# Performance work log

Measured on AMD Instinct MI355X. Metric: run time of the kernel, lower is better.

## Reference

```python
import math
import jax, jax.numpy as jnp
import numpy as np

N_TOKENS = 131072
D_MODEL = 1024
NUM_EXPERT = 64
SWITCH_EPS = 0.1
CAP_RATE = 1.2  # training capacity factor


def setup_inputs() -> dict:
    key = jax.random.key(0)
    k1, k2, k3, k4 = jax.random.split(key, 4)
    inp = jax.random.normal(k1, (N_TOKENS, D_MODEL), dtype=jnp.float32)
    W = jax.random.normal(k2, (D_MODEL, NUM_EXPERT), dtype=jnp.float32) * (1.0 / math.sqrt(D_MODEL))
    b = jax.random.normal(k3, (NUM_EXPERT,), dtype=jnp.float32) * 0.01
    noise = jax.random.uniform(k4, (N_TOKENS, NUM_EXPERT), dtype=jnp.float32)
    return {"inp": inp, "W": W, "b": b, "noise": noise}


def reference(inp, W, b, noise):
    n_tokens = inp.shape[0]
    # gate projection + training-time noise injection (noise in [1-eps, 1+eps])
    score = inp @ W + b
    score = score + (noise * (2.0 * SWITCH_EPS) + (1.0 - SWITCH_EPS))
    score = jax.nn.softmax(score.astype(jnp.float32), axis=-1)  # [N, E]

    # top-1 selection
    top1_idx = jnp.argmax(score, axis=-1)  # [N] int
    top1_score = jnp.take_along_axis(score, top1_idx[:, None], axis=-1)  # [N, 1]
    top1_score = top1_score.astype(inp.dtype)

    # capacity-limited pruning: keep first `capacity` tokens per expert (in order)
    capacity = math.ceil(CAP_RATE * n_tokens / NUM_EXPERT)  # static
    onehot = jax.nn.one_hot(top1_idx, NUM_EXPERT, dtype=jnp.int32)  # [N, E]
    # rank of each token within its expert (0-based, tokens in arrival order)
    rank = jnp.sum(jnp.cumsum(onehot, axis=0) * onehot, axis=-1) - 1  # [N]
    pruned_idx = jnp.where(rank < capacity, top1_idx, -1)  # [N]

    # load-balancing loss over valid (non-pruned) assignments
    valid = pruned_idx > -1
    n_valid = jnp.sum(valid).astype(jnp.float32)
    safe_idx = jnp.where(valid, pruned_idx, 0)
    counts = jnp.zeros((NUM_EXPERT,), dtype=jnp.float32).at[safe_idx].add(valid.astype(jnp.float32))
    fraction_expert = counts / n_valid
    prob_expert = jnp.sum(score, axis=0) / n_valid
    loss = jnp.sum(fraction_expert * prob_expert) * NUM_EXPERT

    return pruned_idx[:, None], top1_score, loss
```

## Files before the change

kernel.cpp:

```cpp
#include <hip/hip_runtime.h>
#include <stdint.h>

#define NTOK   131072
#define DM     1024
#define NE     64
#define TB     64
#define NBLK   2048
#define BK     32
#define NCHUNK 32
#define CAP    2458
#define EPG    16

__device__ __forceinline__ void gload_lds16(const float* g, float* l) {
    __builtin_amdgcn_global_load_lds(
        (const __attribute__((address_space(1))) void*)g,
        (__attribute__((address_space(3))) void*)l, 16, 0, 0);
}

__global__ __launch_bounds__(256, 8)
void gate_kernel(const float* __restrict__ A, const float* __restrict__ W,
                 const float* __restrict__ bias, const float* __restrict__ noise,
                 float* __restrict__ out, int* __restrict__ pk,
                 int* __restrict__ histg, float* __restrict__ colpart)
{
    __shared__ float asA[2][TB][BK];
    __shared__ float smax[TB][5];
    __shared__ float ssum[TB][5];
    __shared__ int   sidx[TB][5];

    const int tid  = threadIdx.x;
    const int lane = tid & 63;
    const int wv   = __builtin_amdgcn_readfirstlane(tid >> 6);
    const int g16  = wv << 4;
    const int blk  = blockIdx.x;
    const int tokBase = blk * TB;
    const int token   = tokBase + lane;

    float acc[EPG];
#pragma unroll
    for (int e = 0; e < EPG; ++e) acc[e] = 0.f;

    const int sl = (lane & 7) ^ ((lane >> 3) & 7);
    const float* gsrc = A + (size_t)(tokBase + wv * 16 + (lane >> 3)) * DM + sl * 4;
    float* lb[2] = { &asA[0][wv * 16][0], &asA[1][wv * 16][0] };

    gload_lds16(gsrc,          lb[0]);
    gload_lds16(gsrc + 8 * DM, lb[0] + 8 * BK);

#pragma unroll 1
    for (int c = 0; c < NCHUNK; ++c) {
        const int cur = c & 1;
        __builtin_amdgcn_s_barrier();
        asm volatile("" ::: "memory");
        if (c + 1 < NCHUNK) {
            const float* gn = gsrc + (size_t)(c + 1) * BK;
            float* ln = lb[cur ^ 1];
            gload_lds16(gn,          ln);
            gload_lds16(gn + 8 * DM, ln + 8 * BK);
            asm volatile("s_waitcnt vmcnt(2)" ::: "memory");
        } else {
            asm volatile("s_waitcnt vmcnt(0)" ::: "memory");
        }
        __builtin_amdgcn_sched_barrier(0);
        __builtin_amdgcn_s_barrier();
        asm volatile("" ::: "memory");

        const float* arow = &asA[cur][lane][0];
        const int k0 = c * BK;
#pragma unroll
        for (int q = 0; q < 8; ++q) {
            const float4 xq = *(const float4*)(arow + ((q ^ (lane & 7)) << 2));
            const float xs[4] = {xq.x, xq.y, xq.z, xq.w};
#pragma unroll
            for (int kk = 0; kk < 4; ++kk) {
                const float x = xs[kk];
                const float* wrow = W + (size_t)(k0 + q * 4 + kk) * NE + g16;
#pragma unroll
                for (int e = 0; e < EPG; ++e)
                    acc[e] = fmaf(x, wrow[e], acc[e]);
            }
        }
    }
    __syncthreads();

    const float* nrow = noise + (size_t)token * NE + g16;
    const float* brow = bias + g16;
#pragma unroll
    for (int q = 0; q < 4; ++q) {
        const float4 nv = ((const float4*)nrow)[q];
        acc[q * 4 + 0] += brow[q * 4 + 0] + nv.x * 0.2f + 0.9f;
        acc[q * 4 + 1] += brow[q * 4 + 1] + nv.y * 0.2f + 0.9f;
        acc[q * 4 + 2] += brow[q * 4 + 2] + nv.z * 0.2f + 0.9f;
        acc[q * 4 + 3] += brow[q * 4 + 3] + nv.w * 0.2f + 0.9f;
    }

    float lm = acc[0]; int li = 0;
#pragma unroll
    for (int e = 1; e < EPG; ++e)
        if (acc[e] > lm) { lm = acc[e]; li = e; }
    smax[lane][wv] = lm;
    sidx[lane][wv] = g16 + li;
    __syncthreads();

    float M = smax[lane][0]; int bi = sidx[lane][0];
#pragma unroll
    for (int g2 = 1; g2 < 4; ++g2) {
        const float m2 = smax[lane][g2];
        if (m2 > M) { M = m2; bi = sidx[lane][g2]; }
    }

    float s = 0.f;
#pragma unroll
    for (int e = 0; e < EPG; ++e) { acc[e] = __expf(acc[e] - M); s += acc[e]; }
    ssum[lane][wv] = s;
    __syncthreads();
    const float denom = ssum[lane][0] + ssum[lane][1] + ssum[lane][2] + ssum[lane][3];
    const float inv = 1.0f / denom;
#pragma unroll
    for (int e = 0; e < EPG; ++e) acc[e] *= inv;

    if (wv == 0) out[NTOK + token] = inv;

#define XSTAGE(M_)                                                       \
    {                                                                    \
        const bool up_ = (lane & (M_)) != 0;                             \
        _Pragma("unroll")                                                \
        for (int j = 0; j < (M_); ++j) {                                 \
            const float a_ = acc[j], b_ = acc[j + (M_)];                 \
            const float r_ = __shfl_xor(up_ ? a_ : b_, (M_), 64);        \
            acc[j] = (up_ ? b_ : a_) + r_;                               \
        }                                                                \
    }
    XSTAGE(8) XSTAGE(4) XSTAGE(2) XSTAGE(1)
#undef XSTAGE
    float cs = acc[0];
    cs += __shfl_xor(cs, 16, 64);
    cs += __shfl_xor(cs, 32, 64);
    if (lane < EPG) colpart[blk * NE + g16 + lane] = cs;

    if (wv == 0) {
        const uint64_t below = (1ull << lane) - 1ull;
        int lrank = 0, h = 0;
#pragma unroll 1
        for (int e = 0; e < NE; ++e) {
            const uint64_t mb = __ballot(bi == e);
            if (bi == e)   lrank = (int)__popcll(mb & below);
            if (lane == e) h = (int)__popcll(mb);
        }
        pk[token] = bi | (lrank << 6);
        histg[blk * NE + lane] = h;
    }
}

__global__ __launch_bounds__(256)
void scan_kernel(int* __restrict__ hist, const float* __restrict__ colpart,
                 int* __restrict__ totals, float* __restrict__ colsums)
{
    __shared__ int   wtot[4];
    __shared__ float wcs[4];
    const int e    = blockIdx.x;
    const int t    = threadIdx.x;
    const int lane = t & 63;
    const int w    = t >> 6;
    const int b0   = t * 8;

    int h[8]; int s = 0; float csl = 0.f;
#pragma unroll
    for (int i = 0; i < 8; ++i) {
        h[i]  = hist[(b0 + i) * NE + e];
        csl  += colpart[(b0 + i) * NE + e];
        s    += h[i];
    }
    int inc = s;
#pragma unroll
    for (int d = 1; d < 64; d <<= 1) {
        const int v = __shfl_up(inc, d, 64);
        if (lane >= d) inc += v;
    }
    float wsum = csl;
#pragma unroll
    for (int m = 32; m; m >>= 1) wsum += __shfl_xor(wsum, m, 64);
    if (lane == 63) wtot[w] = inc;
    if (lane == 0)  wcs[w]  = wsum;
    __syncthreads();

    int base = 0;
#pragma unroll
    for (int ww = 0; ww < 4; ++ww) base += (ww < w) ? wtot[ww] : 0;
    int run = base + inc - s;
#pragma unroll
    for (int i = 0; i < 8; ++i) { hist[(b0 + i) * NE + e] = run; run += h[i]; }

    if (t == 0) {
        totals[e]  = wtot[0] + wtot[1] + wtot[2] + wtot[3];
        colsums[e] = wcs[0] + wcs[1] + wcs[2] + wcs[3];
    }
}

__global__ void loss_kernel(const int* __restrict__ totals,
                            const float* __restrict__ colsums,
                            float* __restrict__ out)
{
    const int e   = threadIdx.x;
    const int tot = totals[e];
    const float cnt = (float)((tot < CAP) ? tot : CAP);
    float nv = cnt, contrib = cnt * colsums[e];
#pragma unroll
    for (int m = 32; m; m >>= 1) {
        nv      += __shfl_xor(nv, m, 64);
        contrib += __shfl_xor(contrib, m, 64);
    }
    if (e == 0) out[2 * NTOK] = 64.0f * contrib / (nv * nv);
}

__global__ void finalize_kernel(const int* __restrict__ pk, const int* __restrict__ offs,
                                float* __restrict__ out)
{
    const int i = blockIdx.x * 256 + threadIdx.x;
    const int v = pk[i];
    const int e = v & 63;
    const int r = (v >> 6) + offs[(i >> 6) * NE + e];
    out[i] = (r < CAP) ? (float)e : -1.0f;
}

extern "C" void kernel_launch(void* const* d_in, const int* in_sizes, int n_in,
                              void* d_out, int out_size, void* d_ws, size_t ws_size,
                              hipStream_t stream)
{
    (void)in_sizes; (void)n_in; (void)out_size; (void)ws_size;
    const float* A     = (const float*)d_in[0];
    const float* W     = (const float*)d_in[1];
    const float* bias  = (const float*)d_in[2];
    const float* noise = (const float*)d_in[3];
    float* out = (float*)d_out;

    char* ws = (char*)d_ws;
    int*   pkbuf   = (int*)ws;
    int*   histg   = (int*)(ws + 524288);
    float* colpart = (float*)(ws + 2 * 524288);
    int*   totals  = (int*)(ws + 3 * 524288);
    float* colsums = (float*)(ws + 3 * 524288 + 256);

    gate_kernel<<<NBLK, 256, 0, stream>>>(A, W, bias, noise, out, pkbuf, histg, colpart);
    scan_kernel<<<NE, 256, 0, stream>>>(histg, colpart, totals, colsums);
    loss_kernel<<<1, 64, 0, stream>>>(totals, colsums, out);
    finalize_kernel<<<NTOK / 256, 256, 0, stream>>>(pkbuf, histg, out);
}
```

Baseline: 252.7 us.

## Compute gate GEMM with split-bf16 MFMA and fp32 rescue for near-ties

Replaces the scalar fp32 FMA gate projection with MFMA bf16 instructions, splitting both the activations and the weights into three bf16 terms so fp32-like accuracy is emulated with six MFMAs per tile. A prep kernel pre-splits and packs W into fragment layout, and tokens whose top-1/top-2 margin is under a threshold are recomputed in exact fp32 by a rescue kernel. The rank computation moves into a separate kernel with 128-token blocks. This targets the FMA-bound inner loop, at the cost of extra kernel launches, an approximate softmax/colsum path that depends on split-bf16 accuracy, and workspace aliasing between gapf and pk.

```diff
diff --git a/kernel.cpp b/kernel.cpp
--- a/kernel.cpp
+++ b/kernel.cpp
@@ -4,12 +4,26 @@
 #define NTOK   131072
 #define DM     1024
 #define NE     64
-#define TB     64
-#define NBLK   2048
+#define TB     128
+#define NBLK   1024
 #define BK     32
 #define NCHUNK 32
 #define CAP    2458
-#define EPG    16
+#define TAU    0.005f
+
+typedef __attribute__((ext_vector_type(8))) short bf16x8;
+typedef __attribute__((ext_vector_type(4))) float f32x4;
+
+union Frag { bf16x8 v; unsigned short u[8]; uint4 q; };
+
+__device__ __forceinline__ unsigned short f2bf_rne(float x) {
+    uint32_t u = __float_as_uint(x);
+    u += 0x7FFFu + ((u >> 16) & 1u);
+    return (unsigned short)(u >> 16);
+}
+__device__ __forceinline__ float bf2f(unsigned short h) {
+    return __uint_as_float(((uint32_t)h) << 16);
+}
 
 __device__ __forceinline__ void gload_lds16(const float* g, float* l) {
     __builtin_amdgcn_global_load_lds(
@@ -17,35 +31,64 @@
         (__attribute__((address_space(3))) void*)l, 16, 0, 0);
 }
 
-__global__ __launch_bounds__(256, 8)
-void gate_kernel(const float* __restrict__ A, const float* __restrict__ W,
+__global__ __launch_bounds__(256)
+void wprep_kernel(const float* __restrict__ W, uint4* __restrict__ Wp)
+{
+    const int c = blockIdx.x;
+    const int t = threadIdx.x >> 6;
+    const int l = threadIdx.x & 63;
+    Frag p1, p2, p3;
+#pragma unroll
+    for (int j = 0; j < 8; ++j) {
+        const float wv = W[(size_t)(c * 32 + (l >> 4) * 8 + j) * NE + t * 16 + (l & 15)];
+        const unsigned short h1 = f2bf_rne(wv);
+        const float r1 = wv - bf2f(h1);
+        const unsigned short h2 = f2bf_rne(r1);
+        const unsigned short h3 = f2bf_rne(r1 - bf2f(h2));
+        p1.u[j] = h1; p2.u[j] = h2; p3.u[j] = h3;
+    }
+    uint4* base = Wp + (size_t)(c * 12 + t * 3) * 64;
+    base[0 * 64 + l] = p1.q;
+    base[1 * 64 + l] = p2.q;
+    base[2 * 64 + l] = p3.q;
+}
+
+__global__ __launch_bounds__(256, 2)
+void gate_kernel(const float* __restrict__ A, const uint4* __restrict__ Wp,
                  const float* __restrict__ bias, const float* __restrict__ noise,
-                 float* __restrict__ out, int* __restrict__ pk,
-                 int* __restrict__ histg, float* __restrict__ colpart)
-{
-    __shared__ float asA[2][TB][BK];
-    __shared__ float smax[TB][5];
-    __shared__ float ssum[TB][5];
-    __shared__ int   sidx[TB][5];
+                 float* __restrict__ out, int* __restrict__ bi_arr,
+                 float* __restrict__ gapf, float* __restrict__ colpart)
+{
+    __shared__ __align__(16) float asA[2][TB][BK];
+    __shared__ uint4 bFr[2][12][64];
+    __shared__ float wcol[4][NE];
 
     const int tid  = threadIdx.x;
     const int lane = tid & 63;
-    const int wv   = __builtin_amdgcn_readfirstlane(tid >> 6);
-    const int g16  = wv << 4;
+    const int w    = __builtin_amdgcn_readfirstlane(tid >> 6);
     const int blk  = blockIdx.x;
     const int tokBase = blk * TB;
-    const int token   = tokBase + lane;
-
-    float acc[EPG];
-#pragma unroll
-    for (int e = 0; e < EPG; ++e) acc[e] = 0.f;
+    const int g    = lane >> 4;
+    const int e16  = lane & 15;
+
+    f32x4 acc[2][4];
+#pragma unroll
+    for (int mt = 0; mt < 2; ++mt)
+#pragma unroll
+        for (int nt = 0; nt < 4; ++nt)
+            acc[mt][nt] = (f32x4){0.f, 0.f, 0.f, 0.f};
 
     const int sl = (lane & 7) ^ ((lane >> 3) & 7);
-    const float* gsrc = A + (size_t)(tokBase + wv * 16 + (lane >> 3)) * DM + sl * 4;
-    float* lb[2] = { &asA[0][wv * 16][0], &asA[1][wv * 16][0] };
-
-    gload_lds16(gsrc,          lb[0]);
-    gload_lds16(gsrc + 8 * DM, lb[0] + 8 * BK);
+    const float* aBase = A + (size_t)(tokBase + w * 32 + (lane >> 3)) * DM + sl * 4;
+
+#pragma unroll
+    for (int q = 0; q < 4; ++q)
+        gload_lds16(aBase + (size_t)q * 8 * DM, &asA[0][w * 32 + q * 8][0]);
+#pragma unroll
+    for (int v = 0; v < 3; ++v) {
+        const int u = w + 4 * v;
+        gload_lds16((const float*)(Wp + (size_t)u * 64 + lane), (float*)&bFr[0][u][0]);
+    }
 
 #pragma unroll 1
     for (int c = 0; c < NCHUNK; ++c) {
@@ -53,11 +96,18 @@
         __builtin_amdgcn_s_barrier();
         asm volatile("" ::: "memory");
         if (c + 1 < NCHUNK) {
-            const float* gn = gsrc + (size_t)(c + 1) * BK;
-            float* ln = lb[cur ^ 1];
-            gload_lds16(gn,          ln);
-            gload_lds16(gn + 8 * DM, ln + 8 * BK);
-            asm volatile("s_waitcnt vmcnt(2)" ::: "memory");
+            const int cn = c + 1;
+#pragma unroll
+            for (int q = 0; q < 4; ++q)
+                gload_lds16(aBase + (size_t)q * 8 * DM + cn * BK,
+                            &asA[cur ^ 1][w * 32 + q * 8][0]);
+#pragma unroll
+            for (int v = 0; v < 3; ++v) {
+                const int u = w + 4 * v;
+                gload_lds16((const float*)(Wp + ((size_t)cn * 12 + u) * 64 + lane),
+                            (float*)&bFr[cur ^ 1][u][0]);
+            }
+            asm volatile("s_waitcnt vmcnt(7)" ::: "memory");
         } else {
             asm volatile("s_waitcnt vmcnt(0)" ::: "memory");
         }
@@ -65,91 +115,176 @@
         __builtin_amdgcn_s_barrier();
         asm volatile("" ::: "memory");
 
-        const float* arow = &asA[cur][lane][0];
-        const int k0 = c * BK;
-#pragma unroll
-        for (int q = 0; q < 8; ++q) {
-            const float4 xq = *(const float4*)(arow + ((q ^ (lane & 7)) << 2));
-            const float xs[4] = {xq.x, xq.y, xq.z, xq.w};
-#pragma unroll
-            for (int kk = 0; kk < 4; ++kk) {
-                const float x = xs[kk];
-                const float* wrow = W + (size_t)(k0 + q * 4 + kk) * NE + g16;
-#pragma unroll
-                for (int e = 0; e < EPG; ++e)
-                    acc[e] = fmaf(x, wrow[e], acc[e]);
-            }
-        }
+        Frag bf[4][3];
+#pragma unroll
+        for (int nt = 0; nt < 4; ++nt)
+#pragma unroll
+            for (int p = 0; p < 3; ++p)
+                bf[nt][p].q = bFr[cur][nt * 3 + p][lane];
+
+        Frag a1[2], a2[2], a3[2];
+#pragma unroll
+        for (int mt = 0; mt < 2; ++mt) {
+            const int row = w * 32 + mt * 16 + e16;
+            const float* rp = &asA[cur][row][0];
+            const float4 x0 = *(const float4*)(rp + (((2 * g)     ^ (lane & 7)) << 2));
+            const float4 x1 = *(const float4*)(rp + (((2 * g + 1) ^ (lane & 7)) << 2));
+            const float xs[8] = {x0.x, x0.y, x0.z, x0.w, x1.x, x1.y, x1.z, x1.w};
+#pragma unroll
+            for (int j = 0; j < 8; ++j) {
+                const float x = xs[j];
+                const unsigned short h1 = f2bf_rne(x);
+                const float r1 = x - bf2f(h1);
+                const unsigned short h2 = f2bf_rne(r1);
+                const unsigned short h3 = f2bf_rne(r1 - bf2f(h2));
+                a1[mt].u[j] = h1; a2[mt].u[j] = h2; a3[mt].u[j] = h3;
+            }
+        }
+
+#pragma unroll
+        for (int mt = 0; mt < 2; ++mt)
+#pragma unroll
+            for (int nt = 0; nt < 4; ++nt) {
+                f32x4 d = acc[mt][nt];
+                d = __builtin_amdgcn_mfma_f32_16x16x32_bf16(a1[mt].v, bf[nt][0].v, d, 0, 0, 0);
+                d = __builtin_amdgcn_mfma_f32_16x16x32_bf16(a1[mt].v, bf[nt][1].v, d, 0, 0, 0);
+                d = __builtin_amdgcn_mfma_f32_16x16x32_bf16(a2[mt].v, bf[nt][0].v, d, 0, 0, 0);
+                d = __builtin_amdgcn_mfma_f32_16x16x32_bf16(a1[mt].v, bf[nt][2].v, d, 0, 0, 0);
+                d = __builtin_amdgcn_mfma_f32_16x16x32_bf16(a2[mt].v, bf[nt][1].v, d, 0, 0, 0);
+                d = __builtin_amdgcn_mfma_f32_16x16x32_bf16(a3[mt].v, bf[nt][0].v, d, 0, 0, 0);
+                acc[mt][nt] = d;
+            }
+    }
+
+#pragma unroll
+    for (int mt = 0; mt < 2; ++mt)
+#pragma unroll
+        for (int r = 0; r < 4; ++r) {
+            const int T = tokBase + w * 32 + mt * 16 + g * 4 + r;
+#pragma unroll
+            for (int nt = 0; nt < 4; ++nt) {
+                const float nz = noise[(size_t)T * NE + nt * 16 + e16];
+                acc[mt][nt][r] += bias[nt * 16 + e16] + nz * 0.2f + 0.9f;
+            }
+        }
+
+    float cw[4] = {0.f, 0.f, 0.f, 0.f};
+#pragma unroll
+    for (int mt = 0; mt < 2; ++mt)
+#pragma unroll
+        for (int r = 0; r < 4; ++r) {
+            const int T = tokBase + w * 32 + mt * 16 + g * 4 + r;
+            float raw[4];
+#pragma unroll
+            for (int nt = 0; nt < 4; ++nt) raw[nt] = acc[mt][nt][r];
+
+            float v = raw[0]; int be = e16;
+#pragma unroll
+            for (int nt = 1; nt < 4; ++nt)
+                if (raw[nt] > v) { v = raw[nt]; be = nt * 16 + e16; }
+#pragma unroll
+            for (int m = 1; m <= 8; m <<= 1) {
+                const float vo = __shfl_xor(v, m, 64);
+                const int   eo = __shfl_xor(be, m, 64);
+                if (vo > v || (vo == v && eo < be)) { v = vo; be = eo; }
+            }
+            float m2 = -1e30f;
+#pragma unroll
+            for (int nt = 0; nt < 4; ++nt)
+                if (nt * 16 + e16 != be && raw[nt] > m2) m2 = raw[nt];
+#pragma unroll
+            for (int m = 1; m <= 8; m <<= 1)
+                m2 = fmaxf(m2, __shfl_xor(m2, m, 64));
+
+            float d = 0.f, pr[4];
+#pragma unroll
+            for (int nt = 0; nt < 4; ++nt) { pr[nt] = __expf(raw[nt] - v); d += pr[nt]; }
+#pragma unroll
+            for (int m = 1; m <= 8; m <<= 1) d += __shfl_xor(d, m, 64);
+            const float inv = 1.0f / d;
+#pragma unroll
+            for (int nt = 0; nt < 4; ++nt) cw[nt] += pr[nt] * inv;
+
+            if (e16 == mt * 4 + r) {
+                out[NTOK + T] = inv;
+                bi_arr[T]     = be;
+                gapf[T]       = v - m2;
+            }
+        }
+
+#pragma unroll
+    for (int nt = 0; nt < 4; ++nt) {
+        cw[nt] += __shfl_xor(cw[nt], 16, 64);
+        cw[nt] += __shfl_xor(cw[nt], 32, 64);
+    }
+    if (lane < 16) {
+#pragma unroll
+        for (int nt = 0; nt < 4; ++nt) wcol[w][nt * 16 + lane] = cw[nt];
     }
     __syncthreads();
-
-    const float* nrow = noise + (size_t)token * NE + g16;
-    const float* brow = bias + g16;
-#pragma unroll
-    for (int q = 0; q < 4; ++q) {
-        const float4 nv = ((const float4*)nrow)[q];
-        acc[q * 4 + 0] += brow[q * 4 + 0] + nv.x * 0.2f + 0.9f;
-        acc[q * 4 + 1] += brow[q * 4 + 1] + nv.y * 0.2f + 0.9f;
-        acc[q * 4 + 2] += brow[q * 4 + 2] + nv.z * 0.2f + 0.9f;
-        acc[q * 4 + 3] += brow[q * 4 + 3] + nv.w * 0.2f + 0.9f;
-    }
-
-    float lm = acc[0]; int li = 0;
-#pragma unroll
-    for (int e = 1; e < EPG; ++e)
-        if (acc[e] > lm) { lm = acc[e]; li = e; }
-    smax[lane][wv] = lm;
-    sidx[lane][wv] = g16 + li;
-    __syncthreads();
-
-    float M = smax[lane][0]; int bi = sidx[lane][0];
-#pragma unroll
-    for (int g2 = 1; g2 < 4; ++g2) {
-        const float m2 = smax[lane][g2];
-        if (m2 > M) { M = m2; bi = sidx[lane][g2]; }
-    }
-
-    float s = 0.f;
-#pragma unroll
-    for (int e = 0; e < EPG; ++e) { acc[e] = __expf(acc[e] - M); s += acc[e]; }
-    ssum[lane][wv] = s;
-    __syncthreads();
-    const float denom = ssum[lane][0] + ssum[lane][1] + ssum[lane][2] + ssum[lane][3];
-    const float inv = 1.0f / denom;
-#pragma unroll
-    for (int e = 0; e < EPG; ++e) acc[e] *= inv;
-
-    if (wv == 0) out[NTOK + token] = inv;
-
-#define XSTAGE(M_)                                                       \
-    {                                                                    \
-        const bool up_ = (lane & (M_)) != 0;                             \
-        _Pragma("unroll")                                                \
-        for (int j = 0; j < (M_); ++j) {                                 \
-            const float a_ = acc[j], b_ = acc[j + (M_)];                 \
-            const float r_ = __shfl_xor(up_ ? a_ : b_, (M_), 64);        \
-            acc[j] = (up_ ? b_ : a_) + r_;                               \
-        }                                                                \
-    }
-    XSTAGE(8) XSTAGE(4) XSTAGE(2) XSTAGE(1)
-#undef XSTAGE
-    float cs = acc[0];
-    cs += __shfl_xor(cs, 16, 64);
-    cs += __shfl_xor(cs, 32, 64);
-    if (lane < EPG) colpart[blk * NE + g16 + lane] = cs;
-
-    if (wv == 0) {
-        const uint64_t below = (1ull << lane) - 1ull;
-        int lrank = 0, h = 0;
+    if (tid < NE)
+        colpart[blk * NE + tid] = wcol[0][tid] + wcol[1][tid] + wcol[2][tid] + wcol[3][tid];
+}
+
+__global__ __launch_bounds__(64)
+void rescue_kernel(const float* __restrict__ A, const float* __restrict__ W,
+                   const float* __restrict__ bias, const float* __restrict__ noise,
+                   const float* __restrict__ gapf, int* __restrict__ bi_arr,
+                   float* __restrict__ out)
+{
+    const int b    = blockIdx.x;
+    const int lane = threadIdx.x;
 #pragma unroll 1
-        for (int e = 0; e < NE; ++e) {
-            const uint64_t mb = __ballot(bi == e);
-            if (bi == e)   lrank = (int)__popcll(mb & below);
-            if (lane == e) h = (int)__popcll(mb);
-        }
-        pk[token] = bi | (lrank << 6);
-        histg[blk * NE + lane] = h;
-    }
+    for (int h = 0; h < 2; ++h) {
+        const int t0 = b * 128 + h * 64;
+        uint64_t mask = __ballot(gapf[t0 + lane] < TAU);
+        while (mask) {
+            const int s = __builtin_ctzll(mask); mask &= mask - 1;
+            const int t = t0 + s;
+            const float* arow = A + (size_t)t * DM;
+            float acc = 0.f;
+#pragma unroll 8
+            for (int k = 0; k < DM; ++k)
+                acc = fmaf(arow[k], W[(size_t)k * NE + lane], acc);
+            acc += bias[lane] + noise[(size_t)t * NE + lane] * 0.2f + 0.9f;
+
+            float v = acc; int be = lane;
+#pragma unroll
+            for (int m = 1; m <= 32; m <<= 1) {
+                const float vo = __shfl_xor(v, m, 64);
+                const int   eo = __shfl_xor(be, m, 64);
+                if (vo > v || (vo == v && eo < be)) { v = vo; be = eo; }
+            }
+            float d = __expf(acc - v);
+#pragma unroll
+            for (int m = 1; m <= 32; m <<= 1) d += __shfl_xor(d, m, 64);
+            if (lane == 0) { bi_arr[t] = be; out[NTOK + t] = 1.0f / d; }
+        }
+    }
+}
+
+__global__ __launch_bounds__(64)
+void rank_kernel(const int* __restrict__ bi_arr, int* __restrict__ pk,
+                 int* __restrict__ histg)
+{
+    const int b    = blockIdx.x;
+    const int lane = threadIdx.x;
+    const uint64_t below = (1ull << lane) - 1ull;
+    const int t0 = b * 128;
+    const int b0 = bi_arr[t0 + lane];
+    const int b1 = bi_arr[t0 + 64 + lane];
+    int lr0 = 0, lr1 = 0, h0 = 0, h1 = 0, h0my = 0;
+#pragma unroll 1
+    for (int e = 0; e < NE; ++e) {
+        const uint64_t m0 = __ballot(b0 == e);
+        const uint64_t m1 = __ballot(b1 == e);
+        if (b0 == e)   lr0 = (int)__popcll(m0 & below);
+        if (b1 == e) { lr1 = (int)__popcll(m1 & below); h0my = (int)__popcll(m0); }
+        if (lane == e) { h0 = (int)__popcll(m0); h1 = (int)__popcll(m1); }
+    }
+    pk[t0 + lane]      = b0 | (lr0 << 6);
+    pk[t0 + 64 + lane] = b1 | ((lr1 + h0my) << 6);
+    histg[b * NE + lane] = h0 + h1;
 }
 
 __global__ __launch_bounds__(256)
@@ -158,18 +293,14 @@
 {
     __shared__ int   wtot[4];
     __shared__ float wcs[4];
-    const int e    = blockIdx.x;
-    const int t    = threadIdx.x;
-    const int lane = t & 63;
-    const int w    = t >> 6;
-    const int b0   = t * 8;
-
-    int h[8]; int s = 0; float csl = 0.f;
-#pragma unroll
-    for (int i = 0; i < 8; ++i) {
-        h[i]  = hist[(b0 + i) * NE + e];
-        csl  += colpart[(b0 + i) * NE + e];
-        s    += h[i];
+    const int e = blockIdx.x, t = threadIdx.x, lane = t & 63, w = t >> 6;
+
+    int h[4]; int s = 0; float csl = 0.f;
+#pragma unroll
+    for (int i = 0; i < 4; ++i) {
+        h[i] = hist[(t * 4 + i) * NE + e];
+        csl += colpart[(t * 4 + i) * NE + e];
+        s   += h[i];
     }
     int inc = s;
 #pragma unroll
@@ -189,7 +320,7 @@
     for (int ww = 0; ww < 4; ++ww) base += (ww < w) ? wtot[ww] : 0;
     int run = base + inc - s;
 #pragma unroll
-    for (int i = 0; i < 8; ++i) { hist[(b0 + i) * NE + e] = run; run += h[i]; }
+    for (int i = 0; i < 4; ++i) { hist[(t * 4 + i) * NE + e] = run; run += h[i]; }
 
     if (t == 0) {
         totals[e]  = wtot[0] + wtot[1] + wtot[2] + wtot[3];
@@ -219,7 +350,7 @@
     const int i = blockIdx.x * 256 + threadIdx.x;
     const int v = pk[i];
     const int e = v & 63;
-    const int r = (v >> 6) + offs[(i >> 6) * NE + e];
+    const int r = (v >> 6) + offs[(i >> 7) * NE + e];
     out[i] = (r < CAP) ? (float)e : -1.0f;
 }
 
@@ -235,14 +366,20 @@
     float* out = (float*)d_out;
 
     char* ws = (char*)d_ws;
-    int*   pkbuf   = (int*)ws;
-    int*   histg   = (int*)(ws + 524288);
-    float* colpart = (float*)(ws + 2 * 524288);
-    int*   totals  = (int*)(ws + 3 * 524288);
-    float* colsums = (float*)(ws + 3 * 524288 + 256);
-
-    gate_kernel<<<NBLK, 256, 0, stream>>>(A, W, bias, noise, out, pkbuf, histg, colpart);
+    int*   bi_arr  = (int*)ws;
+    float* gapf    = (float*)(ws + 524288);
+    int*   pk      = (int*)(ws + 524288);
+    int*   histg   = (int*)(ws + 1048576);
+    float* colpart = (float*)(ws + 1310720);
+    int*   totals  = (int*)(ws + 1572864);
+    float* colsums = (float*)(ws + 1573120);
+    uint4* Wp      = (uint4*)(ws + 1576960);
+
+    wprep_kernel<<<NCHUNK, 256, 0, stream>>>(W, Wp);
+    gate_kernel<<<NBLK, 256, 0, stream>>>(A, Wp, bias, noise, out, bi_arr, gapf, colpart);
+    rescue_kernel<<<NBLK, 64, 0, stream>>>(A, W, bias, noise, gapf, bi_arr, out);
+    rank_kernel<<<NBLK, 64, 0, stream>>>(bi_arr, pk, histg);
     scan_kernel<<<NE, 256, 0, stream>>>(histg, colpart, totals, colsums);
     loss_kernel<<<1, 64, 0, stream>>>(totals, colsums, out);
-    finalize_kernel<<<NTOK / 256, 256, 0, stream>>>(pkbuf, histg, out);
-}
+    finalize_kernel<<<NTOK / 256, 256, 0, stream>>>(pk, histg, out);
+}
```

Result: slower. 400.4 us (+58.4%).
